# Kernel tuning notes

Hardware: AMD Instinct MI355X
Metric: run time of the kernel (lower is better)

## Reference

```python
import jax, jax.numpy as jnp
import numpy as np

C_IN = 256
C_INT = C_IN // 2  # inter_channels


def _conv1x1(x, w, b):
    # x: [B, Cin, H, W], w: [Cout, Cin], b: [Cout]
    return jnp.einsum('bchw,oc->bohw', x, w) + b[None, :, None, None]


def setup_inputs() -> dict:
    key = jax.random.key(0)
    ks = jax.random.split(key, 9)
    B, H, W = 8, 64, 64
    s_in = 1.0 / np.sqrt(C_IN)
    s_int = 1.0 / np.sqrt(C_INT)
    return {
        'x': jax.random.normal(ks[0], (B, C_IN, H, W), dtype=jnp.float32),
        'g_w': jax.random.normal(ks[1], (C_INT, C_IN), dtype=jnp.float32) * s_in,
        'g_b': jax.random.normal(ks[2], (C_INT,), dtype=jnp.float32) * s_in,
        'theta_w': jax.random.normal(ks[3], (C_INT, C_IN), dtype=jnp.float32) * s_in,
        'theta_b': jax.random.normal(ks[4], (C_INT,), dtype=jnp.float32) * s_in,
        'phi_w': jax.random.normal(ks[5], (C_INT, C_IN), dtype=jnp.float32) * s_in,
        'phi_b': jax.random.normal(ks[6], (C_INT,), dtype=jnp.float32) * s_in,
        'W_w': jax.random.normal(ks[7], (C_IN, C_INT), dtype=jnp.float32) * s_int,
        'W_b': jax.random.normal(ks[8], (C_IN,), dtype=jnp.float32) * s_int,
    }


def reference(x, g_w, g_b, theta_w, theta_b, phi_w, phi_b, W_w, W_b):
    B, C, H, W = x.shape
    N = H * W
    g_x = _conv1x1(x, g_w, g_b).reshape(B, C_INT, N)        # [B, Ci, N]
    theta_x = _conv1x1(x, theta_w, theta_b).reshape(B, C_INT, N)
    phi_x = _conv1x1(x, phi_w, phi_b).reshape(B, C_INT, N)
    # f[b, i, j] = theta[:, i] . phi[:, j]  (no scaling, per original)
    f = jnp.einsum('bci,bcj->bij', theta_x, phi_x)          # [B, N, N]
    f_div_C = jax.nn.softmax(f, axis=-1)
    y = jnp.einsum('bij,bcj->bci', f_div_C, g_x)            # [B, Ci, N]
    y = y.reshape(B, C_INT, H, W)
    y = _conv1x1(y, W_w, W_b)                               # [B, C, H, W]
    return x + y
```

## Files before the change

kernel.cpp:

```cpp
#include <hip/hip_runtime.h>

typedef _Float16 f16;
typedef _Float16 f16x4 __attribute__((ext_vector_type(4)));
typedef _Float16 f16x8 __attribute__((ext_vector_type(8)));
typedef __fp16 h2 __attribute__((ext_vector_type(2)));
typedef float f32x4 __attribute__((ext_vector_type(4)));
typedef float f32x16 __attribute__((ext_vector_type(16)));

#define MFMA16(a, b, c) __builtin_amdgcn_mfma_f32_16x16x32_f16(a, b, c, 0, 0, 0)
#define MFMA32(a, b, c) __builtin_amdgcn_mfma_f32_32x32x16_f16(a, b, c, 0, 0, 0)

#if defined(__has_builtin)
#if __has_builtin(__builtin_amdgcn_fdot2)
#define HAS_FDOT2 1
#endif
#endif

typedef const __attribute__((address_space(1))) void gvoid;
typedef __attribute__((address_space(3))) void lvoid;
#define GLDS16(g, l) __builtin_amdgcn_global_load_lds((gvoid*)(g), (lvoid*)(l), 16, 0, 0)

__global__ __launch_bounds__(256) void wcvt_k(
    const float* __restrict__ tw, const float* __restrict__ pw,
    const float* __restrict__ gw, const float* __restrict__ ww,
    f16* __restrict__ Wall, f16* __restrict__ Wepi) {
  int i = blockIdx.x * 256 + threadIdx.x;
  if (i < 384 * 256) {
    int c = i >> 8, cp = i & 255;
    float v = (c < 128) ? tw[c * 256 + cp]
            : (c < 256) ? pw[(c - 128) * 256 + cp]
                        : gw[(c - 256) * 256 + cp];
    Wall[i] = (f16)v;
  }
  int j = i - 384 * 256;
  if (j >= 0 && j < 256 * 128) Wepi[j] = (f16)ww[j];
}

__global__ __launch_bounds__(256) void proj_k(
    const float* __restrict__ x, const f16* __restrict__ Wall,
    const float* __restrict__ tb, const float* __restrict__ pb,
    const float* __restrict__ gb, f16* __restrict__ Q, f16* __restrict__ K,
    f16* __restrict__ Vt) {
  __shared__ f16 xs[64 * 264];
  __shared__ f16 vs[128 * 65];
  int b = blockIdx.x >> 6, nt = blockIdx.x & 63;
  int nbase = nt * 64;
  int tid = threadIdx.x;

  int nq = tid & 15, kq0 = tid >> 4;
#pragma unroll
  for (int p = 0; p < 4; ++p) {
    int kq = kq0 + 16 * p;
    float4 ld[4];
#pragma unroll
    for (int j = 0; j < 4; ++j)
      ld[j] = *(const float4*)(x + ((size_t)b * 256 + 4 * kq + j) * 4096 + nbase + 4 * nq);
#pragma unroll
    for (int e = 0; e < 4; ++e) {
      f16x4 wv = {(f16)((&ld[0].x)[e]), (f16)((&ld[1].x)[e]), (f16)((&ld[2].x)[e]),
                  (f16)((&ld[3].x)[e])};
      *(f16x4*)(&xs[(4 * nq + e) * 264 + 4 * kq]) = wv;
    }
  }
  __syncthreads();

  int w = tid >> 6, lane = tid & 63;
  int lr = lane & 15, lhi = lane >> 4;
  f16x8 a[8];
#pragma unroll
  for (int ks = 0; ks < 8; ++ks)
    a[ks] = *(const f16x8*)(&xs[(w * 16 + lr) * 264 + ks * 32 + lhi * 8]);
  f32x4 acc[24];
#pragma unroll
  for (int ct = 0; ct < 24; ++ct) {
    acc[ct] = {0.f, 0.f, 0.f, 0.f};
    const f16x8* wr = (const f16x8*)(Wall + (size_t)(ct * 16 + lr) * 256);
#pragma unroll
    for (int ks = 0; ks < 8; ++ks) acc[ct] = MFMA16(a[ks], wr[ks * 4 + lhi], acc[ct]);
  }
  int nloc = w * 16 + lhi * 4;
#pragma unroll
  for (int ct = 0; ct < 24; ++ct) {
    int c = ct * 16 + lr;
    float bias = (c < 128) ? tb[c] : (c < 256) ? pb[c - 128] : gb[c - 256];
#pragma unroll
    for (int r = 0; r < 4; ++r) {
      float v = acc[ct][r] + bias;
      int n = nbase + nloc + r;
      if (c < 128)
        Q[((size_t)b * 4096 + n) * 128 + c] = (f16)v;
      else if (c < 256)
        K[((size_t)b * 4096 + n) * 128 + (c - 128)] = (f16)v;
      else
        vs[(c - 256) * 65 + nloc + r] = (f16)v;
    }
  }
  __syncthreads();
  f16* vo = Vt + (size_t)b * 128 * 4096 + nbase;
  for (int rep = 0; rep < 32; ++rep) {
    int idx = rep * 256 + threadIdx.x;
    int c = idx >> 6, j = idx & 63;
    int jp = (j & ~12) | ((j & 4) << 1) | ((j & 8) >> 1);
    vo[(size_t)c * 4096 + jp] = vs[c * 65 + j];
  }
}

__global__ __launch_bounds__(256, 3) void attn_k(const f16* __restrict__ Q,
                                                 const f16* __restrict__ K,
                                                 const f16* __restrict__ Vt,
                                                 f16* __restrict__ Yp,
                                                 float2* __restrict__ ml) {
  __shared__ f16 Ks[2][32 * 128];
  __shared__ f16 Vs[2][128 * 32];
  const float L = 1.44269504f;
  int swzid = ((blockIdx.x & 7) << 7) | ((int)blockIdx.x >> 3);
  int b = swzid >> 7, rem = swzid & 127;
  int qt = rem >> 2, s = rem & 3;
  int qbase = qt * 128;
  int kv0base = s << 10;
  int tid = threadIdx.x;
  int w = tid >> 6, lane = tid & 63;
  int col = lane & 31, hi = lane >> 5;

  const f16* Qr = Q + ((size_t)b * 4096 + qbase + w * 32 + col) * 128;
  f16x8 bq[8];
#pragma unroll
  for (int ks = 0; ks < 8; ++ks) bq[ks] = *(const f16x8*)(Qr + ks * 16 + hi * 8);

  f32x16 yacc[4];
#pragma unroll
  for (int dt = 0; dt < 4; ++dt)
#pragma unroll
    for (int r = 0; r < 16; ++r) yacc[dt][r] = 0.f;
  float lv[4] = {0.f, 0.f, 0.f, 0.f};
  float m = -1e30f, nmL = 1e30f;

  unsigned koff[2], voff[2];
#pragma unroll
  for (int c = 0; c < 2; ++c) {
    koff[c] = (unsigned)((lane >> 1) * 256 + (w * 4 + c * 2 + (lane & 1)) * 16);
    voff[c] = (unsigned)((w * 32 + (lane >> 1)) * 8192 + (c * 2 + (lane & 1)) * 16);
  }
  const char* KbB = (const char*)(K + (size_t)b * 4096 * 128);
  const char* VbB = (const char*)(Vt + (size_t)b * 128 * 4096);
  char* KsB = (char*)&Ks[0][0];
  char* VsB = (char*)&Vs[0][0];

  auto stage = [&](int t, int buf) {
    int kv0 = kv0base + t * 32;
    const char* kb = KbB + (size_t)kv0 * 256;
    const char* vb = VbB + (size_t)kv0 * 2;
    char* kl = KsB + buf * 8192 + w * 2048;
    char* vl = VsB + buf * 8192 + w * 2048;
#pragma unroll
    for (int c = 0; c < 2; ++c) {
      GLDS16(kb + koff[c], kl + c * 1024);
      GLDS16(vb + voff[c], vl + c * 1024);
    }
  };

  int lanebase = col * 32 + hi * 16;

  stage(0, 0);

  for (int t = 0; t < 32; ++t) {
    int cur = t & 1;
    __syncthreads();
    if (t + 1 < 32) stage(t + 1, cur ^ 1);

    f32x16 s2;
#pragma unroll
    for (int r = 0; r < 16; ++r) s2[r] = 0.f;
    __builtin_amdgcn_s_setprio(1);
    {
      const char* kcur = KsB + cur * 8192 + lanebase;
#pragma unroll
      for (int ks = 0; ks < 8; ++ks) {
        f16x8 ak = *(const f16x8*)(kcur + ks * 1024);
        s2 = MFMA32(ak, bq[ks], s2);
      }
    }
    __builtin_amdgcn_s_setprio(0);

    float a0 = fmaxf(fmaxf(s2[0], s2[1]), s2[2]);
    float a1 = fmaxf(fmaxf(s2[3], s2[4]), s2[5]);
    float a2 = fmaxf(fmaxf(s2[6], s2[7]), s2[8]);
    float a3 = fmaxf(fmaxf(s2[9], s2[10]), s2[11]);
    float a4 = fmaxf(fmaxf(s2[12], s2[13]), s2[14]);
    float pm = fmaxf(fmaxf(fmaxf(a0, a1), fmaxf(a2, a3)), fmaxf(a4, s2[15]));
    pm = fmaxf(pm, __shfl_xor(pm, 32));
    if (pm > m + 8.f) {
      float sc = __expf(m - pm);
      m = pm;
      nmL = -m * L;
#pragma unroll
      for (int i = 0; i < 4; ++i) lv[i] *= sc;
#pragma unroll
      for (int dt = 0; dt < 4; ++dt)
#pragma unroll
        for (int r = 0; r < 16; ++r) yacc[dt][r] *= sc;
    }
#pragma unroll
    for (int r = 0; r < 16; ++r) s2[r] = exp2f(fmaf(s2[r], L, nmL));

    f16x8 pfrA, pfrB;
#pragma unroll
    for (int c = 0; c < 8; ++c) {
      pfrA[c] = (f16)s2[c];
      pfrB[c] = (f16)s2[8 + c];
    }
#if defined(HAS_FDOT2)
    {
      h2 one2 = {1.0f, 1.0f};
      const h2* pa = (const h2*)&pfrA;
      const h2* pb2 = (const h2*)&pfrB;
#pragma unroll
      for (int j = 0; j < 4; ++j) {
        lv[j] = __builtin_amdgcn_fdot2(pa[j], one2, lv[j], false);
        lv[j] = __builtin_amdgcn_fdot2(pb2[j], one2, lv[j], false);
      }
    }
#else
#pragma unroll
    for (int j = 0; j < 4; ++j)
      lv[j] += (float)pfrA[2 * j] + (float)pfrA[2 * j + 1] + (float)pfrB[2 * j] +
               (float)pfrB[2 * j + 1];
#endif

    __builtin_amdgcn_s_setprio(1);
    {
      const char* vcur = VsB + cur * 8192 + lanebase;
#pragma unroll
      for (int dt = 0; dt < 4; ++dt) {
        f16x8 av0 = *(const f16x8*)(vcur + dt * 2048);
        yacc[dt] = MFMA32(av0, pfrA, yacc[dt]);
        f16x8 av1 = *(const f16x8*)(vcur + dt * 2048 + 1024);
        yacc[dt] = MFMA32(av1, pfrB, yacc[dt]);
      }
    }
    __builtin_amdgcn_s_setprio(0);
  }

  float l = (lv[0] + lv[1]) + (lv[2] + lv[3]);
  l += __shfl_xor(l, 32);

  int rowG = b * 4096 + qbase + w * 32 + col;
  f16* yo = Yp + ((size_t)s * 32768 + rowG) * 128;
  float inv = 1.0f / l;
#pragma unroll
  for (int dt = 0; dt < 4; ++dt)
#pragma unroll
    for (int a = 0; a < 4; ++a) {
      f16x4 ov = {(f16)(yacc[dt][4 * a] * inv), (f16)(yacc[dt][4 * a + 1] * inv),
                  (f16)(yacc[dt][4 * a + 2] * inv), (f16)(yacc[dt][4 * a + 3] * inv)};
      *(f16x4*)(yo + dt * 32 + a * 8 + hi * 4) = ov;
    }
  if (hi == 0) ml[s * 32768 + rowG] = make_float2(m, l);
}

__global__ __launch_bounds__(256) void epi_k(const f16* __restrict__ Yp,
                                             const float2* __restrict__ ml,
                                             const f16* __restrict__ Wepi,
                                             const float* __restrict__ Wb,
                                             const float* __restrict__ x,
                                             float* __restrict__ out) {
  int b = blockIdx.x >> 6, nt = blockIdx.x & 63;
  int nbase = nt * 64;
  int w = threadIdx.x >> 6, lane = threadIdx.x & 63;
  int lr = lane & 15, lhi = lane >> 4;
  f16x8 by[4][4];
#pragma unroll
  for (int n4 = 0; n4 < 4; ++n4) {
    int row = b * 4096 + nbase + n4 * 16 + lr;
    float2 m0 = ml[row], m1 = ml[32768 + row], m2 = ml[65536 + row], m3 = ml[98304 + row];
    float mm = fmaxf(fmaxf(m0.x, m1.x), fmaxf(m2.x, m3.x));
    float w0 = m0.y * __expf(m0.x - mm), w1 = m1.y * __expf(m1.x - mm);
    float w2 = m2.y * __expf(m2.x - mm), w3 = m3.y * __expf(m3.x - mm);
    float inv = 1.f / (w0 + w1 + w2 + w3);
    w0 *= inv; w1 *= inv; w2 *= inv; w3 *= inv;
    size_t rb = (size_t)row * 128;
#pragma unroll
    for (int ks = 0; ks < 4; ++ks) {
      int eo = ks * 32 + lhi * 8;
      f16x8 a0 = *(const f16x8*)(Yp + rb + eo);
      f16x8 a1 = *(const f16x8*)(Yp + (size_t)32768 * 128 + rb + eo);
      f16x8 a2 = *(const f16x8*)(Yp + (size_t)65536 * 128 + rb + eo);
      f16x8 a3 = *(const f16x8*)(Yp + (size_t)98304 * 128 + rb + eo);
      f16x8 o;
#pragma unroll
      for (int e = 0; e < 8; ++e)
        o[e] = (f16)(w0 * (float)a0[e] + w1 * (float)a1[e] + w2 * (float)a2[e] +
                     w3 * (float)a3[e]);
      by[n4][ks] = o;
    }
  }
#pragma unroll
  for (int ot = 0; ot < 4; ++ot) {
    int o0 = w * 64 + ot * 16;
    const f16x8* wr = (const f16x8*)(Wepi + (size_t)(o0 + lr) * 128);
    f16x8 a[4];
#pragma unroll
    for (int ks = 0; ks < 4; ++ks) a[ks] = wr[ks * 4 + lhi];
#pragma unroll
    for (int n4 = 0; n4 < 4; ++n4) {
      f32x4 acc = {0.f, 0.f, 0.f, 0.f};
#pragma unroll
      for (int ks = 0; ks < 4; ++ks) acc = MFMA16(a[ks], by[n4][ks], acc);
#pragma unroll
      for (int r = 0; r < 4; ++r) {
        int o = o0 + lhi * 4 + r;
        int n = nbase + n4 * 16 + lr;
        size_t idx = ((size_t)b * 256 + o) * 4096 + n;
        out[idx] = x[idx] + Wb[o] + acc[r];
      }
    }
  }
}

extern "C" void kernel_launch(void* const* d_in, const int* in_sizes, int n_in,
                              void* d_out, int out_size, void* d_ws, size_t ws_size,
                              hipStream_t stream) {
  const float* x       = (const float*)d_in[0];
  const float* g_w     = (const float*)d_in[1];
  const float* g_b     = (const float*)d_in[2];
  const float* theta_w = (const float*)d_in[3];
  const float* theta_b = (const float*)d_in[4];
  const float* phi_w   = (const float*)d_in[5];
  const float* phi_b   = (const float*)d_in[6];
  const float* W_w     = (const float*)d_in[7];
  const float* W_b     = (const float*)d_in[8];
  float* out = (float*)d_out;

  f16* Q    = (f16*)d_ws;
  f16* Kk   = Q + (size_t)8 * 4096 * 128;
  f16* Vt   = Kk + (size_t)8 * 4096 * 128;
  f16* Wall = Vt + (size_t)8 * 4096 * 128;
  f16* Wepi = Wall + 384 * 256;
  float2* ml = (float2*)(Wepi + 256 * 128);
  f16* Yp   = (f16*)(ml + 4 * 32768);

  wcvt_k<<<512, 256, 0, stream>>>(theta_w, phi_w, g_w, W_w, Wall, Wepi);
  proj_k<<<512, 256, 0, stream>>>(x, Wall, theta_b, phi_b, g_b, Q, Kk, Vt);
  attn_k<<<1024, 256, 0, stream>>>(Q, Kk, Vt, Yp, ml);
  epi_k<<<512, 256, 0, stream>>>(Yp, ml, Wepi, W_b, x, out);
}
```

Baseline: 195.6 us.

## Pre-tile K and V in LDS order so attention loads are contiguous

The projection kernel now writes K and V^T into a tiled global layout: each 32-key tile is stored as one contiguous 8 KB block, already permuted into the order the attention kernel's shared-memory staging expects. The attention kernel's direct global-to-LDS loads then become fully contiguous 16-byte-per-lane streams, replacing the strided gathers that used to pull from rows 256 bytes or 8 KB apart. This is meant to improve coalescing and DRAM/L2 efficiency in the attention loop. The cost is scattered, non-contiguous stores in the projection epilogue, and the layout is tightly coupled between the two kernels.

```diff
diff --git a/kernel.cpp b/kernel.cpp
--- a/kernel.cpp
+++ b/kernel.cpp
@@ -87,21 +87,28 @@
     for (int r = 0; r < 4; ++r) {
       float v = acc[ct][r] + bias;
       int n = nbase + nloc + r;
-      if (c < 128)
+      if (c < 128) {
         Q[((size_t)b * 4096 + n) * 128 + c] = (f16)v;
-      else if (c < 256)
-        K[((size_t)b * 4096 + n) * 128 + (c - 128)] = (f16)v;
-      else
+      } else if (c < 256) {
+        int d = c - 128;
+        int slot = ((d >> 4) << 6) + ((n & 31) << 1) + ((d >> 3) & 1);
+        K[(size_t)b * 524288 + (size_t)(n >> 5) * 4096 + slot * 8 + (d & 7)] = (f16)v;
+      } else {
         vs[(c - 256) * 65 + nloc + r] = (f16)v;
+      }
     }
   }
   __syncthreads();
-  f16* vo = Vt + (size_t)b * 128 * 4096 + nbase;
+  f16* vo = Vt + (size_t)b * 524288;
   for (int rep = 0; rep < 32; ++rep) {
-    int idx = rep * 256 + threadIdx.x;
+    int idx = rep * 256 + tid;
     int c = idx >> 6, j = idx & 63;
-    int jp = (j & ~12) | ((j & 4) << 1) | ((j & 8) >> 1);
-    vo[(size_t)c * 4096 + jp] = vs[c * 65 + j];
+    int n = nbase + j;
+    int nl = j & 31;
+    int p = (nl & 3) | ((nl & 4) << 1) | ((nl & 8) >> 1) | (nl & 16);
+    int g = p >> 3, e = p & 7;
+    int slot = ((c >> 5) << 7) + ((g >> 1) << 6) + ((c & 31) << 1) + (g & 1);
+    vo[(size_t)(n >> 5) * 4096 + slot * 8 + e] = vs[c * 65 + j];
   }
 }
 
@@ -117,7 +124,7 @@
   int b = swzid >> 7, rem = swzid & 127;
   int qt = rem >> 2, s = rem & 3;
   int qbase = qt * 128;
-  int kv0base = s << 10;
+  int tile0 = s * 32;
   int tid = threadIdx.x;
   int w = tid >> 6, lane = tid & 63;
   int col = lane & 31, hi = lane >> 5;
@@ -135,27 +142,21 @@
   float lv[4] = {0.f, 0.f, 0.f, 0.f};
   float m = -1e30f, nmL = 1e30f;
 
-  unsigned koff[2], voff[2];
-#pragma unroll
-  for (int c = 0; c < 2; ++c) {
-    koff[c] = (unsigned)((lane >> 1) * 256 + (w * 4 + c * 2 + (lane & 1)) * 16);
-    voff[c] = (unsigned)((w * 32 + (lane >> 1)) * 8192 + (c * 2 + (lane & 1)) * 16);
-  }
-  const char* KbB = (const char*)(K + (size_t)b * 4096 * 128);
-  const char* VbB = (const char*)(Vt + (size_t)b * 128 * 4096);
+  const char* KbB = (const char*)(K + (size_t)b * 524288);
+  const char* VbB = (const char*)(Vt + (size_t)b * 524288);
   char* KsB = (char*)&Ks[0][0];
   char* VsB = (char*)&Vs[0][0];
 
   auto stage = [&](int t, int buf) {
-    int kv0 = kv0base + t * 32;
-    const char* kb = KbB + (size_t)kv0 * 256;
-    const char* vb = VbB + (size_t)kv0 * 2;
+    size_t tb_ = (size_t)(tile0 + t) * 8192;
+    const char* kb = KbB + tb_ + w * 2048 + lane * 16;
+    const char* vb = VbB + tb_ + w * 2048 + lane * 16;
     char* kl = KsB + buf * 8192 + w * 2048;
     char* vl = VsB + buf * 8192 + w * 2048;
 #pragma unroll
     for (int c = 0; c < 2; ++c) {
-      GLDS16(kb + koff[c], kl + c * 1024);
-      GLDS16(vb + voff[c], vl + c * 1024);
+      GLDS16(kb + c * 1024, kl + c * 1024);
+      GLDS16(vb + c * 1024, vl + c * 1024);
     }
   };
 
```

After: 190.5 us. 2.6% less time.
